# Kernel tuning notes

Hardware: AMD Instinct MI355X
Metric: run time of the kernel (lower is better)

## Reference

```python
import jax, jax.numpy as jnp
import numpy as np

B, N, E_PER, DIN, DOUT = 64, 1024, 16384, 128, 128
NN, E = B * N, B * E_PER
K = int(0.5 * N)  # TopKPooling ratio=0.5, fixed per-graph node count
EPS_BN = 1e-5


def setup_inputs():
    key = jax.random.key(0)
    ks = jax.random.split(key, 16)
    x = jax.random.normal(ks[0], (NN, DIN), jnp.float32)
    # edges constrained within each graph (offset + local index)
    offs = jnp.repeat(jnp.arange(B, dtype=jnp.int32) * N, E_PER)
    src = offs + jax.random.randint(ks[1], (E,), 0, N, dtype=jnp.int32)
    dst = offs + jax.random.randint(ks[2], (E,), 0, N, dtype=jnp.int32)
    edge_index = jnp.stack([src, dst])  # [2, E]
    edge_attr = jax.random.normal(ks[3], (E, DIN), jnp.float32)
    batch_idx = jnp.repeat(jnp.arange(B, dtype=jnp.int32), N)
    s = 1.0 / np.sqrt(DIN)
    Wq = jax.random.normal(ks[4], (DIN, DOUT), jnp.float32) * s
    bq = jnp.zeros((DOUT,), jnp.float32)
    Wk = jax.random.normal(ks[5], (DIN, DOUT), jnp.float32) * s
    bk = jnp.zeros((DOUT,), jnp.float32)
    Wv = jax.random.normal(ks[6], (DIN, DOUT), jnp.float32) * s
    bv = jnp.zeros((DOUT,), jnp.float32)
    We = jax.random.normal(ks[7], (DIN, DOUT), jnp.float32) * s
    be = jnp.zeros((DOUT,), jnp.float32)
    Ws = jax.random.normal(ks[8], (DIN, DOUT), jnp.float32) * s  # root/skip weight
    bs = jnp.zeros((DOUT,), jnp.float32)
    pool_w = jax.random.normal(ks[9], (DOUT,), jnp.float32)
    gamma = jnp.ones((DOUT,), jnp.float32)
    beta = jnp.zeros((DOUT,), jnp.float32)
    return {"x": x, "edge_index": edge_index, "edge_attr": edge_attr,
            "batch_idx": batch_idx, "Wq": Wq, "bq": bq, "Wk": Wk, "bk": bk,
            "Wv": Wv, "bv": bv, "We": We, "be": be, "Ws": Ws, "bs": bs,
            "pool_w": pool_w, "gamma": gamma, "beta": beta}


def reference(x, edge_index, edge_attr, batch_idx, Wq, bq, Wk, bk, Wv, bv,
              We, be, Ws, bs, pool_w, gamma, beta):
    src, dst = edge_index[0], edge_index[1]
    # ---- TransformerConv (heads=1, concat) ----
    q = x @ Wq + bq                      # [NN, D]
    k = x @ Wk + bk
    v = x @ Wv + bv
    e = edge_attr @ We + be              # [E, D]
    ke = k[src] + e
    alpha = jnp.sum(q[dst] * ke, axis=-1) / jnp.sqrt(jnp.float32(DOUT))  # [E]
    # segment softmax over incoming edges of each dst node
    m = jax.ops.segment_max(alpha, dst, num_segments=NN)
    ex = jnp.exp(alpha - m[dst])
    denom = jax.ops.segment_sum(ex, dst, num_segments=NN)
    attn = ex / (denom[dst] + 1e-16)
    msg = attn[:, None] * (v[src] + e)   # [E, D]
    out = jax.ops.segment_sum(msg, dst, num_segments=NN)
    out = out + (x @ Ws + bs)            # root weight (skip)
    out = jax.nn.relu(out)
    # ---- TopKPooling ----
    score = jnp.tanh(out @ pool_w / jnp.linalg.norm(pool_w))  # [NN]
    top_s, top_i = jax.lax.top_k(score.reshape(B, N), K)      # [B, K]
    offs = (jnp.arange(B, dtype=top_i.dtype) * N)[:, None]
    perm = (top_i + offs).reshape(-1)                          # [B*K] global ids
    xp = out[perm] * top_s.reshape(-1)[:, None]                # [B*K, D]
    batch_out = jnp.repeat(jnp.arange(B, dtype=jnp.int32), K)
    # remap / filter edges: keep edges with both endpoints kept
    node_map = jnp.full((NN,), -1, dtype=jnp.int32).at[perm].set(
        jnp.arange(B * K, dtype=jnp.int32))
    ns, nd = node_map[src], node_map[dst]
    valid = (ns >= 0) & (nd >= 0)                              # [E] edge mask
    new_edge_index = jnp.where(valid[None, :], jnp.stack([ns, nd]), -1)
    new_edge_attr = edge_attr * valid[:, None].astype(edge_attr.dtype)
    # ---- BatchNorm1d (training: batch stats, biased variance) ----
    mu = jnp.mean(xp, axis=0)
    var = jnp.mean(jnp.square(xp - mu), axis=0)
    y = gamma * (xp - mu) * jax.lax.rsqrt(var + EPS_BN) + beta
    return (y, new_edge_index, new_edge_attr, batch_out, valid)
```

## Files before the change

### kernel.cpp

```cpp
#include <hip/hip_runtime.h>
#include <cstddef>
#include <cstdint>

#define NODES 65536
#define NEDGE 1048576
#define NB    64
#define NPER  1024
#define TOPK  512
#define BKR   32768
#define DIM   128
#define NM    ((size_t)NODES * DIM)

typedef float f32x4 __attribute__((ext_vector_type(4)));

__device__ __forceinline__ f32x4 ntload4(const f32x4* p) {
  return __builtin_nontemporal_load(p);
}
__device__ __forceinline__ void ntstore4(f32x4* p, f32x4 v) {
  __builtin_nontemporal_store(v, p);
}
__device__ __forceinline__ long long ntloadll(const long long* p) {
  return __builtin_nontemporal_load(p);
}
__device__ __forceinline__ float dotv(f32x4 a, f32x4 b) {
  return fmaf(a.x, b.x, fmaf(a.y, b.y, fmaf(a.z, b.z, a.w * b.w)));
}

template <int CTRL>
__device__ __forceinline__ float dpp_addf(float x) {
  const int y = __builtin_amdgcn_update_dpp(0, __float_as_int(x), CTRL, 0xF, 0xF, true);
  return x + __int_as_float(y);
}
__device__ __forceinline__ float row16_sum(float x) {
  x = dpp_addf<0xB1>(x);
  x = dpp_addf<0x4E>(x);
  x = dpp_addf<0x124>(x);
  x = dpp_addf<0x128>(x);
  return x;
}

__device__ __forceinline__ void gemm_core(
    const float* __restrict__ A, const f32x4* __restrict__ sW,
    const float* __restrict__ bias, float* __restrict__ Out,
    size_t row0, int ostride, int tc) {
  const float* a0 = A + row0 * 128;
  f32x4 acc0[8], acc1[8];
#pragma unroll
  for (int r = 0; r < 8; ++r) { acc0[r] = (f32x4)(0.f); acc1[r] = (f32x4)(0.f); }
#pragma unroll 4
  for (int k4 = 0; k4 < 32; ++k4) {
    f32x4 a[8];
#pragma unroll
    for (int r = 0; r < 8; ++r)
      a[r] = *reinterpret_cast<const f32x4*>(a0 + r * 128 + k4 * 4);
#pragma unroll
    for (int kk = 0; kk < 4; ++kk) {
      const f32x4 w0 = sW[(k4 * 4 + kk) * 32 + tc * 2];
      const f32x4 w1 = sW[(k4 * 4 + kk) * 32 + tc * 2 + 1];
#pragma unroll
      for (int r = 0; r < 8; ++r) {
        const float av = a[r][kk];
        acc0[r] += av * w0;
        acc1[r] += av * w1;
      }
    }
  }
  const f32x4 b0 = reinterpret_cast<const f32x4*>(bias)[tc * 2];
  const f32x4 b1 = reinterpret_cast<const f32x4*>(bias)[tc * 2 + 1];
#pragma unroll
  for (int r = 0; r < 8; ++r) {
    f32x4* outp = reinterpret_cast<f32x4*>(Out + (row0 + r) * (size_t)ostride + tc * 8);
    outp[0] = acc0[r] + b0;
    outp[1] = acc1[r] + b1;
  }
}

__global__ __launch_bounds__(512) void gemm_multi(
    const float* __restrict__ x,
    const float* __restrict__ Wq, const float* __restrict__ bq, float* __restrict__ q,
    const float* __restrict__ Wk, const float* __restrict__ bk,
    const float* __restrict__ Wv, const float* __restrict__ bv, float* __restrict__ kv,
    const float* __restrict__ Wc, const float* __restrict__ bc, float* __restrict__ qw) {
  __shared__ f32x4 sW[128 * 32];
  const int which = blockIdx.x >> 8;
  const int bid = blockIdx.x & 255;
  const int t = threadIdx.x;
  const float* W; const float* bias; float* Out; int ostride = 128;
  if (which == 0)      { W = Wq; bias = bq; Out = q; }
  else if (which == 1) { W = Wk; bias = bk; Out = kv;       ostride = 256; }
  else if (which == 2) { W = Wv; bias = bv; Out = kv + 128; ostride = 256; }
  else                 { W = Wc; bias = bc; Out = qw; }
  const f32x4* W4 = reinterpret_cast<const f32x4*>(W);
#pragma unroll
  for (int i = 0; i < 8; ++i) sW[t + i * 512] = W4[t + i * 512];
  __syncthreads();
  gemm_core(x, sW, bias, Out, (size_t)bid * 256 + (t >> 4) * 8, ostride, t & 15);
}

__global__ __launch_bounds__(256) void gemm_final2(
    const float* __restrict__ agge, const float* __restrict__ We,
    const float* __restrict__ x,    const float* __restrict__ Ws,
    const float* __restrict__ be,   const float* __restrict__ bs,
    const float* __restrict__ aggv, const float* __restrict__ pwn,
    float* __restrict__ outc, float* __restrict__ score) {
  __shared__ f32x4 sW[128 * 32];
  const int t = threadIdx.x;
  const int tc = t & 15;
  const size_t row0 = (size_t)blockIdx.x * 128 + (t >> 4) * 8;
  f32x4 acc0[8], acc1[8];
#pragma unroll
  for (int r = 0; r < 8; ++r) { acc0[r] = (f32x4)(0.f); acc1[r] = (f32x4)(0.f); }

#pragma unroll
  for (int phase = 0; phase < 2; ++phase) {
    const float* W = phase ? Ws : We;
    const float* A = phase ? x : agge;
    const f32x4* W4 = reinterpret_cast<const f32x4*>(W);
    if (phase) __syncthreads();
#pragma unroll
    for (int i = 0; i < 16; ++i) sW[t + i * 256] = W4[t + i * 256];
    __syncthreads();
    const float* a0 = A + row0 * 128;
#pragma unroll 4
    for (int k4 = 0; k4 < 32; ++k4) {
      f32x4 a[8];
#pragma unroll
      for (int r = 0; r < 8; ++r)
        a[r] = *reinterpret_cast<const f32x4*>(a0 + r * 128 + k4 * 4);
#pragma unroll
      for (int kk = 0; kk < 4; ++kk) {
        const f32x4 w0 = sW[(k4 * 4 + kk) * 32 + tc * 2];
        const f32x4 w1 = sW[(k4 * 4 + kk) * 32 + tc * 2 + 1];
#pragma unroll
        for (int r = 0; r < 8; ++r) {
          const float av = a[r][kk];
          acc0[r] += av * w0;
          acc1[r] += av * w1;
        }
      }
    }
  }
  const f32x4 b0 = reinterpret_cast<const f32x4*>(be)[tc * 2] +
                   reinterpret_cast<const f32x4*>(bs)[tc * 2];
  const f32x4 b1 = reinterpret_cast<const f32x4*>(be)[tc * 2 + 1] +
                   reinterpret_cast<const f32x4*>(bs)[tc * 2 + 1];
  const f32x4 p0 = reinterpret_cast<const f32x4*>(pwn)[tc * 2];
  const f32x4 p1 = reinterpret_cast<const f32x4*>(pwn)[tc * 2 + 1];
#pragma unroll
  for (int r = 0; r < 8; ++r) {
    const f32x4 v0 = reinterpret_cast<const f32x4*>(aggv + (row0 + r) * 128 + tc * 8)[0];
    const f32x4 v1 = reinterpret_cast<const f32x4*>(aggv + (row0 + r) * 128 + tc * 8)[1];
    f32x4 o0 = acc0[r] + b0 + v0;
    f32x4 o1 = acc1[r] + b1 + v1;
#pragma unroll
    for (int c = 0; c < 4; ++c) { o0[c] = fmaxf(o0[c], 0.f); o1[c] = fmaxf(o1[c], 0.f); }
    f32x4* outp = reinterpret_cast<f32x4*>(outc + (row0 + r) * 128 + tc * 8);
    outp[0] = o0; outp[1] = o1;
    float sp = dotv(o0, p0) + dotv(o1, p1);
#pragma unroll
    for (int d = 1; d < 16; d <<= 1) sp += __shfl_xor(sp, d, 16);
    if (tc == 0) score[row0 + r] = tanhf(sp);
  }
}

__global__ __launch_bounds__(256) void setup_kernel(
    const float* __restrict__ pool_w, float* __restrict__ pwn,
    const float* __restrict__ Wq, const float* __restrict__ bq,
    const float* __restrict__ We, float* __restrict__ Wc, float* __restrict__ bc,
    int* __restrict__ deg, int* __restrict__ nmap, float* __restrict__ bn2) {
  const int blk = blockIdx.x;
  const int t = threadIdx.x;
  if (blk < 256) {
    const int i = blk * 256 + t;
    deg[i] = 0; nmap[i] = -1;
    if (i < 256) bn2[i] = 0.f;
  } else if (blk == 256) {
    __shared__ float red[128];
    if (t < 128) {
      const float vv = pool_w[t];
      red[t] = vv * vv;
    }
    __syncthreads();
    for (int d = 64; d > 0; d >>= 1) {
      if (t < d) red[t] += red[t + d];
      __syncthreads();
    }
    if (t < 128) pwn[t] = pool_w[t] * rsqrtf(red[0]);
  } else {
    __shared__ float sWe[2][128];
    const int i = (blk - 257) * 2 + (t >> 7);
    const int tl = t & 127;
    sWe[t >> 7][tl] = We[i * 128 + tl];
    __syncthreads();
    float s = 0.f;
    for (int d = 0; d < 128; ++d) s = fmaf(Wq[tl * 128 + d], sWe[t >> 7][d], s);
    Wc[tl * 128 + i] = s;
    if (tl == 0) {
      float sb = 0.f;
      for (int d = 0; d < 128; ++d) sb = fmaf(bq[d], sWe[t >> 7][d], sb);
      bc[i] = sb;
    }
  }
}

__global__ void deg_kernel(const int* __restrict__ dst, int* __restrict__ deg) {
  const int e = blockIdx.x * 256 + threadIdx.x;
  atomicAdd(&deg[dst[e]], 1);
}

__global__ __launch_bounds__(1024) void scan_kernel(const int* __restrict__ deg,
                                                    int* __restrict__ offs,
                                                    int* __restrict__ woff) {
  __shared__ int part[1024];
  const int t = threadIdx.x;
  const int base = t * 64;
  int s = 0;
  for (int j = 0; j < 64; ++j) s += deg[base + j];
  part[t] = s;
  __syncthreads();
  for (int d = 1; d < 1024; d <<= 1) {
    const int add = (t >= d) ? part[t - d] : 0;
    __syncthreads();
    part[t] += add;
    __syncthreads();
  }
  int run = part[t] - s;
  for (int j = 0; j < 64; ++j) {
    offs[base + j] = run; woff[base + j] = run;
    run += deg[base + j];
  }
  if (t == 1023) offs[NODES] = run;
}

__global__ void scatter_kernel(const int* __restrict__ dst, const int* __restrict__ src,
                               int* __restrict__ woff, long long* __restrict__ srt) {
  const int e = blockIdx.x * 256 + threadIdx.x;
  const int pos = atomicAdd(&woff[dst[e]], 1);
  srt[pos] = ((long long)src[e] << 32) | (unsigned)e;
}

__global__ __launch_bounds__(256) void attn_v7(
    const float* __restrict__ q, const float* __restrict__ kv,
    const float* __restrict__ qw, const float* __restrict__ ea,
    const float* __restrict__ be, const long long* __restrict__ srt,
    const int* __restrict__ offs, float* __restrict__ aggv,
    float* __restrict__ agge) {
  int b = blockIdx.x;
  b = (b & 7) * 2048 + (b >> 3);
  const int wid = b * 4 + (threadIdx.x >> 6);
  const int lane = threadIdx.x & 63;
  const int g = lane >> 4;
  const int l = lane & 15;
  const f32x4* q4  = reinterpret_cast<const f32x4*>(q)  + (size_t)wid * 32;
  const f32x4* qw4 = reinterpret_cast<const f32x4*>(qw) + (size_t)wid * 32;
  const f32x4* be4 = reinterpret_cast<const f32x4*>(be);
  const f32x4 qv0 = q4[2 * l],  qv1 = q4[2 * l + 1];
  const f32x4 qwv0 = qw4[2 * l], qwv1 = qw4[2 * l + 1];
  const float SCALE = 0.08838834764831845f;
  const float qbeS = row16_sum(dotv(qv0, be4[2 * l]) + dotv(qv1, be4[2 * l + 1])) * SCALE;

  const f32x4* kv4 = reinterpret_cast<const f32x4*>(kv);
  const f32x4* ea4 = reinterpret_cast<const f32x4*>(ea);
  float denom = 0.f;
  f32x4 av0 = (f32x4)(0.f), av1 = (f32x4)(0.f), ag0 = (f32x4)(0.f), ag1 = (f32x4)(0.f);
  const int e0 = offs[wid], e1 = offs[wid + 1];
  int p = e0 + g;
  long long pkA = 0, pkB = 0;
  if (p < e1) {
    pkA = ntloadll(srt + p);
    pkB = ((p + 4) < e1) ? ntloadll(srt + p + 4) : pkA;
  }
  while (p < e1) {
    const bool h2 = (p + 4) < e1;
    const int pn = p + 8;
    long long nA = 0, nB = 0;
    if (pn < e1) {
      nA = ntloadll(srt + pn);
      nB = ((pn + 4) < e1) ? ntloadll(srt + pn + 4) : nA;
    }
    const int eA = (int)pkA, sA = (int)(pkA >> 32);
    const int eB = (int)pkB, sB = (int)(pkB >> 32);
    const f32x4* kvA = kv4 + (size_t)sA * 64 + 2 * l;
    const f32x4* kvB = kv4 + (size_t)sB * 64 + 2 * l;
    const f32x4 kA0 = kvA[0], kA1 = kvA[1], vA0 = kvA[32], vA1 = kvA[33];
    const f32x4 kB0 = kvB[0], kB1 = kvB[1], vB0 = kvB[32], vB1 = kvB[33];
    const f32x4 fA0 = ntload4(ea4 + (size_t)eA * 32 + 2 * l);
    const f32x4 fA1 = ntload4(ea4 + (size_t)eA * 32 + 2 * l + 1);
    const f32x4 fB0 = ntload4(ea4 + (size_t)eB * 32 + 2 * l);
    const f32x4 fB1 = ntload4(ea4 + (size_t)eB * 32 + 2 * l + 1);
    float pA = dotv(qv0, kA0) + dotv(qv1, kA1) + dotv(qwv0, fA0) + dotv(qwv1, fA1);
    float pB = dotv(qv0, kB0) + dotv(qv1, kB1) + dotv(qwv0, fB0) + dotv(qwv1, fB1);
    pA = row16_sum(pA);
    pB = row16_sum(pB);
    const float wA = __expf(fmaf(pA, SCALE, qbeS));
    const float wB = h2 ? __expf(fmaf(pB, SCALE, qbeS)) : 0.f;
    denom += wA + wB;
    av0 += wA * vA0 + wB * vB0;
    av1 += wA * vA1 + wB * vB1;
    ag0 += wA * fA0 + wB * fB0;
    ag1 += wA * fA1 + wB * fB1;
    pkA = nA; pkB = nB; p = pn;
  }
#pragma unroll
  for (int d = 16; d < 64; d <<= 1) {
    denom += __shfl_xor(denom, d, 64);
#pragma unroll
    for (int c = 0; c < 4; ++c) {
      av0[c] += __shfl_xor(av0[c], d, 64);
      av1[c] += __shfl_xor(av1[c], d, 64);
      ag0[c] += __shfl_xor(ag0[c], d, 64);
      ag1[c] += __shfl_xor(ag1[c], d, 64);
    }
  }
  if (g == 0) {
    const float inv = 1.f / (denom + 1e-16f);
    f32x4* aggv4 = reinterpret_cast<f32x4*>(aggv) + (size_t)wid * 32;
    f32x4* agge4 = reinterpret_cast<f32x4*>(agge) + (size_t)wid * 32;
    aggv4[2 * l]     = av0 * inv;
    aggv4[2 * l + 1] = av1 * inv;
    agge4[2 * l]     = ag0 * inv;
    agge4[2 * l + 1] = ag1 * inv;
  }
}

__global__ __launch_bounds__(1024) void topk_kernel(
    const float* __restrict__ score, int* __restrict__ perm,
    float* __restrict__ tops, float* __restrict__ batchf, int* __restrict__ nmap) {
  __shared__ float ss[1024];
  __shared__ int si[1024];
  const int b = blockIdx.x, t = threadIdx.x;
  ss[t] = score[b * 1024 + t];
  si[t] = t;
  __syncthreads();
  for (int size = 2; size <= 1024; size <<= 1) {
    for (int stride = size >> 1; stride > 0; stride >>= 1) {
      const int j = t ^ stride;
      if (j > t) {
        const float s1 = ss[t], s2 = ss[j];
        const int i1 = si[t], i2 = si[j];
        const bool bj = (s2 > s1) || (s2 == s1 && i2 < i1);
        const bool dir = ((t & size) == 0);
        if (dir ? bj : !bj) { ss[t] = s2; ss[j] = s1; si[t] = i2; si[j] = i1; }
      }
      __syncthreads();
    }
  }
  if (t < TOPK) {
    const int g = b * TOPK + t;
    perm[g] = b * 1024 + si[t];
    tops[g] = ss[t];
    batchf[g] = (float)b;
    nmap[b * 1024 + si[t]] = g;
  }
}

__global__ __launch_bounds__(128) void xp_kernel(
    const float* __restrict__ outc, const int* __restrict__ perm,
    const float* __restrict__ tops, float* __restrict__ y,
    float* __restrict__ bnsum, float* __restrict__ bnsq) {
  const int t = threadIdx.x;
  const int r0 = blockIdx.x * 128;
  float s = 0.f, s2 = 0.f;
  for (int i = 0; i < 128; ++i) {
    const int r = r0 + i;
    const int g = perm[r];
    const float val = outc[(size_t)g * DIM + t] * tops[r];
    y[(size_t)r * DIM + t] = val;
    s += val;
    s2 = fmaf(val, val, s2);
  }
  atomicAdd(&bnsum[t], s);
  atomicAdd(&bnsq[t], s2);
}

__global__ __launch_bounds__(256) void bnapply_v2(
    float* __restrict__ y, const float* __restrict__ bnsum, const float* __restrict__ bnsq,
    const float* __restrict__ gamma, const float* __restrict__ beta) {
  const size_t i4 = (size_t)blockIdx.x * 256 + threadIdx.x;
  const int c4 = (int)(i4 & 31);
  f32x4 a, c;
#pragma unroll
  for (int j = 0; j < 4; ++j) {
    const int col = c4 * 4 + j;
    const float mu = bnsum[col] * (1.f / BKR);
    const float var = bnsq[col] * (1.f / BKR) - mu * mu;
    const float aa = gamma[col] * rsqrtf(var + 1e-5f);
    a[j] = aa;
    c[j] = beta[col] - mu * aa;
  }
  f32x4 v = reinterpret_cast<f32x4*>(y)[i4];
#pragma unroll
  for (int j = 0; j < 4; ++j) v[j] = fmaf(v[j], a[j], c[j]);
  reinterpret_cast<f32x4*>(y)[i4] = v;
}

__global__ __launch_bounds__(256) void efnea_kernel(
    const int* __restrict__ srcArr, const int* __restrict__ dstArr,
    const int* __restrict__ nm, const float* __restrict__ ea,
    float* __restrict__ nei, float* __restrict__ validf, float* __restrict__ nea) {
  const int row = blockIdx.x * 8 + (threadIdx.x >> 5);
  const int lane = threadIdx.x & 31;
  const int ns = nm[srcArr[row]];
  const int nd = nm[dstArr[row]];
  const bool val = (ns >= 0) && (nd >= 0);
  if (lane == 0) {
    nei[row] = val ? (float)ns : -1.f;
    nei[NEDGE + row] = val ? (float)nd : -1.f;
    validf[row] = val ? 1.f : 0.f;
  }
  const size_t i4 = (size_t)row * 32 + lane;
  f32x4 v = (f32x4)(0.f);
  if (val) v = ntload4(reinterpret_cast<const f32x4*>(ea) + i4);
  ntstore4(reinterpret_cast<f32x4*>(nea) + i4, v);
}

extern "C" void kernel_launch(void* const* d_in, const int* in_sizes, int n_in,
                              void* d_out, int out_size, void* d_ws, size_t ws_size,
                              hipStream_t stream) {
  const float* x     = (const float*)d_in[0];
  const int*   eidx  = (const int*)d_in[1];
  const float* eattr = (const float*)d_in[2];
  const float* Wq = (const float*)d_in[4];  const float* bq = (const float*)d_in[5];
  const float* Wk = (const float*)d_in[6];  const float* bk = (const float*)d_in[7];
  const float* Wv = (const float*)d_in[8];  const float* bv = (const float*)d_in[9];
  const float* We = (const float*)d_in[10]; const float* be = (const float*)d_in[11];
  const float* Ws = (const float*)d_in[12]; const float* bs = (const float*)d_in[13];
  const float* pool_w = (const float*)d_in[14];
  const float* gamma  = (const float*)d_in[15];
  const float* beta   = (const float*)d_in[16];

  const int* srcArr = eidx;
  const int* dstArr = eidx + NEDGE;

  float* out = (float*)d_out;
  float* y      = out;
  float* nei    = out + (size_t)BKR * DIM;
  float* nea    = nei + 2 * (size_t)NEDGE;
  float* batchf = nea + (size_t)NEDGE * DIM;
  float* validf = batchf + BKR;

  float* q    = nea + 0 * NM;
  float* kv   = nea + 1 * NM;
  float* qw   = nea + 3 * NM;
  float* aggv = nea + 4 * NM;
  float* agge = nea + 5 * NM;
  float* outc = nea + 6 * NM;

  char* w = (char*)d_ws;
  size_t off = 0;
  float* score= (float*)(w + off); off += (size_t)NODES * 4;
  float* pwn  = (float*)(w + off); off += 128 * 4;
  float* Wc   = (float*)(w + off); off += 128 * 128 * 4;
  float* bc   = (float*)(w + off); off += 128 * 4;
  float* tops = (float*)(w + off); off += (size_t)BKR * 4;
  float* bnsum= (float*)(w + off); off += 128 * 4;
  float* bnsq = (float*)(w + off); off += 128 * 4;
  int* deg    = (int*)(w + off); off += (size_t)NODES * 4;
  int* offs   = (int*)(w + off); off += ((size_t)NODES + 8) * 4;
  int* woff   = (int*)(w + off); off += (size_t)NODES * 4;
  int* nmap   = (int*)(w + off); off += (size_t)NODES * 4;
  int* perm   = (int*)(w + off); off += (size_t)BKR * 4;
  long long* srt = (long long*)(w + off); off += (size_t)NEDGE * 8;

  setup_kernel<<<321, 256, 0, stream>>>(pool_w, pwn, Wq, bq, We, Wc, bc,
                                        deg, nmap, (float*)bnsum);

  gemm_multi<<<4 * 256, 512, 0, stream>>>(
      x, Wq, bq, q, Wk, bk, Wv, bv, kv, Wc, bc, qw);

  deg_kernel<<<NEDGE / 256, 256, 0, stream>>>(dstArr, deg);
  scan_kernel<<<1, 1024, 0, stream>>>(deg, offs, woff);
  scatter_kernel<<<NEDGE / 256, 256, 0, stream>>>(dstArr, srcArr, woff, srt);

  attn_v7<<<NODES / 4, 256, 0, stream>>>(q, kv, qw, eattr, be, srt, offs, aggv, agge);

  gemm_final2<<<NODES / 128, 256, 0, stream>>>(agge, We, x, Ws, be, bs, aggv, pwn,
                                               outc, score);

  topk_kernel<<<NB, 1024, 0, stream>>>(score, perm, tops, batchf, nmap);

  xp_kernel<<<BKR / 128, 128, 0, stream>>>(outc, perm, tops, y, bnsum, bnsq);
  bnapply_v2<<<(BKR * 32) / 256, 256, 0, stream>>>(y, bnsum, bnsq, gamma, beta);

  efnea_kernel<<<NEDGE / 8, 256, 0, stream>>>(srcArr, dstArr, nmap, eattr, nei, validf, nea);
}
```

Baseline: 724.7 us.

## Fuse setup, CSR build and projections into one kernel; fuse top-k with gather

The separate deg/scan/scatter kernels become a per-graph CSR build using shared-memory atomics and a block scan, which relies on edges being contiguous per graph. That build runs inside the same launch as the Q/K/V/Wc projection GEMMs and the init work, so global atomics on the degree array and the single-block scan disappear. Top-k is fused with the xp gather and BN partial sums so perm and tops no longer round-trip through memory. Wc now comes from a dedicated small kernel that must finish before the mega kernel. The risk is fewer launches being traded for heterogeneous blocks, and the per-graph CSR layout assuming the test's edge ordering.

```diff
diff --git a/kernel.cpp b/kernel.cpp
--- a/kernel.cpp
+++ b/kernel.cpp
@@ -39,6 +39,26 @@
   return x;
 }
 
+__global__ __launch_bounds__(512) void wc_kernel(
+    const float* __restrict__ Wq, const float* __restrict__ bq,
+    const float* __restrict__ We, float* __restrict__ Wc, float* __restrict__ bc) {
+  __shared__ float sWe[4][128];
+  const int t = threadIdx.x;
+  const int sub = t >> 7;
+  const int tl = t & 127;
+  const int i = blockIdx.x * 4 + sub;
+  sWe[sub][tl] = We[i * 128 + tl];
+  __syncthreads();
+  float s = 0.f;
+  for (int d = 0; d < 128; ++d) s = fmaf(Wq[tl * 128 + d], sWe[sub][d], s);
+  Wc[tl * 128 + i] = s;
+  if (tl == 0) {
+    float sb = 0.f;
+    for (int d = 0; d < 128; ++d) sb = fmaf(bq[d], sWe[sub][d], sb);
+    bc[i] = sb;
+  }
+}
+
 __device__ __forceinline__ void gemm_core(
     const float* __restrict__ A, const f32x4* __restrict__ sW,
     const float* __restrict__ bias, float* __restrict__ Out,
@@ -75,26 +95,89 @@
   }
 }
 
-__global__ __launch_bounds__(512) void gemm_multi(
+__global__ __launch_bounds__(512) void mega_kernel(
     const float* __restrict__ x,
     const float* __restrict__ Wq, const float* __restrict__ bq, float* __restrict__ q,
     const float* __restrict__ Wk, const float* __restrict__ bk,
     const float* __restrict__ Wv, const float* __restrict__ bv, float* __restrict__ kv,
-    const float* __restrict__ Wc, const float* __restrict__ bc, float* __restrict__ qw) {
-  __shared__ f32x4 sW[128 * 32];
-  const int which = blockIdx.x >> 8;
-  const int bid = blockIdx.x & 255;
+    const float* __restrict__ Wc, const float* __restrict__ bc, float* __restrict__ qw,
+    const int* __restrict__ srcArr, const int* __restrict__ dstArr,
+    int* __restrict__ offs, long long* __restrict__ srt,
+    const float* __restrict__ pool_w, float* __restrict__ pwn,
+    int* __restrict__ nmap, float* __restrict__ bn2) {
+  __shared__ __align__(16) char smem[65536];
+  const int blk = blockIdx.x;
   const int t = threadIdx.x;
-  const float* W; const float* bias; float* Out; int ostride = 128;
-  if (which == 0)      { W = Wq; bias = bq; Out = q; }
-  else if (which == 1) { W = Wk; bias = bk; Out = kv;       ostride = 256; }
-  else if (which == 2) { W = Wv; bias = bv; Out = kv + 128; ostride = 256; }
-  else                 { W = Wc; bias = bc; Out = qw; }
-  const f32x4* W4 = reinterpret_cast<const f32x4*>(W);
-#pragma unroll
-  for (int i = 0; i < 8; ++i) sW[t + i * 512] = W4[t + i * 512];
-  __syncthreads();
-  gemm_core(x, sW, bias, Out, (size_t)bid * 256 + (t >> 4) * 8, ostride, t & 15);
+
+  if (blk < 1024) {
+    f32x4* sW = reinterpret_cast<f32x4*>(smem);
+    const int which = blk >> 8;
+    const int bid = blk & 255;
+    const float* W; const float* bias; float* Out; int ostride = 128;
+    if (which == 0)      { W = Wq; bias = bq; Out = q; }
+    else if (which == 1) { W = Wk; bias = bk; Out = kv;       ostride = 256; }
+    else if (which == 2) { W = Wv; bias = bv; Out = kv + 128; ostride = 256; }
+    else                 { W = Wc; bias = bc; Out = qw; }
+    const f32x4* W4 = reinterpret_cast<const f32x4*>(W);
+#pragma unroll
+    for (int i = 0; i < 8; ++i) sW[t + i * 512] = W4[t + i * 512];
+    __syncthreads();
+    gemm_core(x, sW, bias, Out, (size_t)bid * 256 + (t >> 4) * 8, ostride, t & 15);
+  } else if (blk < 1088) {
+    int* cnt = reinterpret_cast<int*>(smem);
+    int* aux = cnt + 1024;
+    const int g = blk - 1024;
+    const int ebase = g * 16384;
+    cnt[t] = 0; cnt[t + 512] = 0;
+    __syncthreads();
+#pragma unroll 4
+    for (int j = 0; j < 32; ++j) {
+      const int e = ebase + j * 512 + t;
+      atomicAdd(&cnt[dstArr[e] & 1023], 1);
+    }
+    __syncthreads();
+    const int two0 = cnt[2 * t], two1 = cnt[2 * t + 1];
+    const int part = two0 + two1;
+    aux[t] = part;
+    __syncthreads();
+    for (int d = 1; d < 512; d <<= 1) {
+      const int add = (t >= d) ? aux[t - d] : 0;
+      __syncthreads();
+      aux[t] += add;
+      __syncthreads();
+    }
+    const int excl2 = aux[t] - part;
+    __syncthreads();
+    offs[g * 1024 + 2 * t]     = ebase + excl2;
+    offs[g * 1024 + 2 * t + 1] = ebase + excl2 + two0;
+    cnt[2 * t] = excl2;
+    cnt[2 * t + 1] = excl2 + two0;
+    if (g == 0 && t == 0) offs[NODES] = NEDGE;
+    __syncthreads();
+#pragma unroll 4
+    for (int j = 0; j < 32; ++j) {
+      const int e = ebase + j * 512 + t;
+      const int d = dstArr[e] & 1023;
+      const int pos = atomicAdd(&cnt[d], 1);
+      srt[ebase + pos] = ((long long)srcArr[e] << 32) | (unsigned)e;
+    }
+  } else if (blk < 1120) {
+    const int base = ((blk - 1088) * 512 + t) * 4;
+    nmap[base] = -1; nmap[base + 1] = -1; nmap[base + 2] = -1; nmap[base + 3] = -1;
+    if (blk == 1088 && t < 256) bn2[t] = 0.f;
+  } else {
+    float* red = reinterpret_cast<float*>(smem);
+    if (t < 128) {
+      const float vv = pool_w[t];
+      red[t] = vv * vv;
+    }
+    __syncthreads();
+    for (int d = 64; d > 0; d >>= 1) {
+      if (t < d) red[t] += red[t + d];
+      __syncthreads();
+    }
+    if (t < 128) pwn[t] = pool_w[t] * rsqrtf(red[0]);
+  }
 }
 
 __global__ __launch_bounds__(256) void gemm_final2(
@@ -161,82 +244,6 @@
     for (int d = 1; d < 16; d <<= 1) sp += __shfl_xor(sp, d, 16);
     if (tc == 0) score[row0 + r] = tanhf(sp);
   }
-}
-
-__global__ __launch_bounds__(256) void setup_kernel(
-    const float* __restrict__ pool_w, float* __restrict__ pwn,
-    const float* __restrict__ Wq, const float* __restrict__ bq,
-    const float* __restrict__ We, float* __restrict__ Wc, float* __restrict__ bc,
-    int* __restrict__ deg, int* __restrict__ nmap, float* __restrict__ bn2) {
-  const int blk = blockIdx.x;
-  const int t = threadIdx.x;
-  if (blk < 256) {
-    const int i = blk * 256 + t;
-    deg[i] = 0; nmap[i] = -1;
-    if (i < 256) bn2[i] = 0.f;
-  } else if (blk == 256) {
-    __shared__ float red[128];
-    if (t < 128) {
-      const float vv = pool_w[t];
-      red[t] = vv * vv;
-    }
-    __syncthreads();
-    for (int d = 64; d > 0; d >>= 1) {
-      if (t < d) red[t] += red[t + d];
-      __syncthreads();
-    }
-    if (t < 128) pwn[t] = pool_w[t] * rsqrtf(red[0]);
-  } else {
-    __shared__ float sWe[2][128];
-    const int i = (blk - 257) * 2 + (t >> 7);
-    const int tl = t & 127;
-    sWe[t >> 7][tl] = We[i * 128 + tl];
-    __syncthreads();
-    float s = 0.f;
-    for (int d = 0; d < 128; ++d) s = fmaf(Wq[tl * 128 + d], sWe[t >> 7][d], s);
-    Wc[tl * 128 + i] = s;
-    if (tl == 0) {
-      float sb = 0.f;
-      for (int d = 0; d < 128; ++d) sb = fmaf(bq[d], sWe[t >> 7][d], sb);
-      bc[i] = sb;
-    }
-  }
-}
-
-__global__ void deg_kernel(const int* __restrict__ dst, int* __restrict__ deg) {
-  const int e = blockIdx.x * 256 + threadIdx.x;
-  atomicAdd(&deg[dst[e]], 1);
-}
-
-__global__ __launch_bounds__(1024) void scan_kernel(const int* __restrict__ deg,
-                                                    int* __restrict__ offs,
-                                                    int* __restrict__ woff) {
-  __shared__ int part[1024];
-  const int t = threadIdx.x;
-  const int base = t * 64;
-  int s = 0;
-  for (int j = 0; j < 64; ++j) s += deg[base + j];
-  part[t] = s;
-  __syncthreads();
-  for (int d = 1; d < 1024; d <<= 1) {
-    const int add = (t >= d) ? part[t - d] : 0;
-    __syncthreads();
-    part[t] += add;
-    __syncthreads();
-  }
-  int run = part[t] - s;
-  for (int j = 0; j < 64; ++j) {
-    offs[base + j] = run; woff[base + j] = run;
-    run += deg[base + j];
-  }
-  if (t == 1023) offs[NODES] = run;
-}
-
-__global__ void scatter_kernel(const int* __restrict__ dst, const int* __restrict__ src,
-                               int* __restrict__ woff, long long* __restrict__ srt) {
-  const int e = blockIdx.x * 256 + threadIdx.x;
-  const int pos = atomicAdd(&woff[dst[e]], 1);
-  srt[pos] = ((long long)src[e] << 32) | (unsigned)e;
 }
 
 __global__ __launch_bounds__(256) void attn_v7(
@@ -323,9 +330,10 @@
   }
 }
 
-__global__ __launch_bounds__(1024) void topk_kernel(
-    const float* __restrict__ score, int* __restrict__ perm,
-    float* __restrict__ tops, float* __restrict__ batchf, int* __restrict__ nmap) {
+__global__ __launch_bounds__(1024) void topkxp_kernel(
+    const float* __restrict__ score, const float* __restrict__ outc,
+    float* __restrict__ y, float* __restrict__ batchf, int* __restrict__ nmap,
+    float* __restrict__ bnsum, float* __restrict__ bnsq) {
   __shared__ float ss[1024];
   __shared__ int si[1024];
   const int b = blockIdx.x, t = threadIdx.x;
@@ -346,31 +354,23 @@
     }
   }
   if (t < TOPK) {
-    const int g = b * TOPK + t;
-    perm[g] = b * 1024 + si[t];
-    tops[g] = ss[t];
-    batchf[g] = (float)b;
-    nmap[b * 1024 + si[t]] = g;
-  }
-}
-
-__global__ __launch_bounds__(128) void xp_kernel(
-    const float* __restrict__ outc, const int* __restrict__ perm,
-    const float* __restrict__ tops, float* __restrict__ y,
-    float* __restrict__ bnsum, float* __restrict__ bnsq) {
-  const int t = threadIdx.x;
-  const int r0 = blockIdx.x * 128;
+    batchf[b * TOPK + t] = (float)b;
+    nmap[b * 1024 + si[t]] = b * TOPK + t;
+  }
+  __syncthreads();
+  const int c = t & 127;
+  const int rbase = t >> 7;
   float s = 0.f, s2 = 0.f;
-  for (int i = 0; i < 128; ++i) {
-    const int r = r0 + i;
-    const int g = perm[r];
-    const float val = outc[(size_t)g * DIM + t] * tops[r];
-    y[(size_t)r * DIM + t] = val;
+  for (int i = 0; i < 64; ++i) {
+    const int r = rbase + 8 * i;
+    const int gnode = b * 1024 + si[r];
+    const float val = outc[(size_t)gnode * DIM + c] * ss[r];
+    y[((size_t)b * TOPK + r) * DIM + c] = val;
     s += val;
     s2 = fmaf(val, val, s2);
   }
-  atomicAdd(&bnsum[t], s);
-  atomicAdd(&bnsq[t], s2);
+  atomicAdd(&bnsum[c], s);
+  atomicAdd(&bnsq[c], s2);
 }
 
 __global__ __launch_bounds__(256) void bnapply_v2(
@@ -452,34 +452,25 @@
   float* pwn  = (float*)(w + off); off += 128 * 4;
   float* Wc   = (float*)(w + off); off += 128 * 128 * 4;
   float* bc   = (float*)(w + off); off += 128 * 4;
-  float* tops = (float*)(w + off); off += (size_t)BKR * 4;
   float* bnsum= (float*)(w + off); off += 128 * 4;
   float* bnsq = (float*)(w + off); off += 128 * 4;
-  int* deg    = (int*)(w + off); off += (size_t)NODES * 4;
   int* offs   = (int*)(w + off); off += ((size_t)NODES + 8) * 4;
-  int* woff   = (int*)(w + off); off += (size_t)NODES * 4;
   int* nmap   = (int*)(w + off); off += (size_t)NODES * 4;
-  int* perm   = (int*)(w + off); off += (size_t)BKR * 4;
   long long* srt = (long long*)(w + off); off += (size_t)NEDGE * 8;
 
-  setup_kernel<<<321, 256, 0, stream>>>(pool_w, pwn, Wq, bq, We, Wc, bc,
-                                        deg, nmap, (float*)bnsum);
-
-  gemm_multi<<<4 * 256, 512, 0, stream>>>(
-      x, Wq, bq, q, Wk, bk, Wv, bv, kv, Wc, bc, qw);
-
-  deg_kernel<<<NEDGE / 256, 256, 0, stream>>>(dstArr, deg);
-  scan_kernel<<<1, 1024, 0, stream>>>(deg, offs, woff);
-  scatter_kernel<<<NEDGE / 256, 256, 0, stream>>>(dstArr, srcArr, woff, srt);
+  wc_kernel<<<32, 512, 0, stream>>>(Wq, bq, We, Wc, bc);
+
+  mega_kernel<<<1121, 512, 0, stream>>>(
+      x, Wq, bq, q, Wk, bk, Wv, bv, kv, Wc, bc, qw,
+      srcArr, dstArr, offs, srt, pool_w, pwn, nmap, (float*)bnsum);
 
   attn_v7<<<NODES / 4, 256, 0, stream>>>(q, kv, qw, eattr, be, srt, offs, aggv, agge);
 
   gemm_final2<<<NODES / 128, 256, 0, stream>>>(agge, We, x, Ws, be, bs, aggv, pwn,
                                                outc, score);
 
-  topk_kernel<<<NB, 1024, 0, stream>>>(score, perm, tops, batchf, nmap);
-
-  xp_kernel<<<BKR / 128, 128, 0, stream>>>(outc, perm, tops, y, bnsum, bnsq);
+  topkxp_kernel<<<NB, 1024, 0, stream>>>(score, outc, y, batchf, nmap, bnsum, bnsq);
+
   bnapply_v2<<<(BKR * 32) / 256, 256, 0, stream>>>(y, bnsum, bnsq, gamma, beta);
 
   efnea_kernel<<<NEDGE / 8, 256, 0, stream>>>(srcArr, dstArr, nmap, eattr, nei, validf, nea);
```

Result: faster. 641.4 us (-11.5%).
